# Optimization experiments

Measured on AMD Instinct MI355X. Metric: run time of the kernel, lower is better.

## Reference

```python
import jax, jax.numpy as jnp
import numpy as np

N_GENES_TOTAL = 2000
N_FREQ = 50
E_DIM = 10
N_FRAGMENTS = 131072
N_CELLS = 200
N_GENES_MB = 500
ENC_DIM = 4 * N_FREQ  # 200


def setup_inputs() -> dict:
    key = jax.random.key(0)
    k0, k1, k2, k3 = jax.random.split(key, 4)
    # fragment coordinates (start/end positions around the TSS, ~kb scale)
    coordinates = jax.random.normal(k0, (N_FRAGMENTS, 2), dtype=jnp.float32) * 1000.0
    # sorted ragged cell-x-gene segment index (required by segment_*_coo)
    local_cellxgene_ix = jnp.sort(
        jax.random.randint(k1, (N_FRAGMENTS,), 0, N_CELLS * N_GENES_MB)
    )
    # genes of interest in this minibatch (indices into the global gene table)
    genes_oi = jax.random.randint(k2, (N_GENES_MB,), 0, N_GENES_TOTAL)
    # consistent per-fragment gene mapping
    genemapping = genes_oi[local_cellxgene_ix % N_GENES_MB]
    # FragmentEmbedder params
    stdv = 1.0 / np.sqrt(E_DIM)
    W1 = jax.random.uniform(k3, (N_GENES_TOTAL, ENC_DIM, E_DIM), dtype=jnp.float32,
                            minval=-stdv, maxval=stdv)
    b1 = jnp.zeros((N_GENES_TOTAL, E_DIM), dtype=jnp.float32)
    # EmbeddingToExpression params, 'default' init: first 5 ones, rest zero, last -1
    w2 = np.zeros((N_GENES_TOTAL, E_DIM), dtype=np.float32)
    w2[:, :5] = 1.0
    w2[:, -1] = -1.0
    w2 = jnp.asarray(w2)
    b2 = jnp.zeros((N_GENES_TOTAL,), dtype=jnp.float32)
    return dict(coordinates=coordinates, genemapping=genemapping,
                local_cellxgene_ix=local_cellxgene_ix, genes_oi=genes_oi,
                W1=W1, b1=b1, w2=w2, b2=b2, cell_n=N_CELLS, gene_n=N_GENES_MB)


def _sine_encode(coordinates):
    nf = N_FREQ
    i = jnp.arange(1, nf + 1, dtype=coordinates.dtype)
    freqs = jnp.repeat(1.0 / (1000.0 ** (2.0 * i / nf)), 2)            # [2*nf]
    shifts = jnp.tile(jnp.array([0.0, jnp.pi / 2], coordinates.dtype), nf)  # [2*nf]
    # [F,2,1]*[2nf] -> [F,2,2nf] -> flatten last two -> [F, 4*nf]
    enc = jnp.sin((coordinates[..., None] * freqs + shifts)
                  .reshape(coordinates.shape[0], -1))
    return enc


def reference(coordinates, genemapping, local_cellxgene_ix, genes_oi,
              W1, b1, w2, b2, cell_n, gene_n):
    # FragmentEmbedder: sine encoding + per-gene linear + sigmoid
    enc = _sine_encode(coordinates)                                   # [F, 200]
    h = jnp.einsum('fe,feo->fo', enc, W1[genemapping]) + b1[genemapping]  # [F, 10]
    h = jax.nn.sigmoid(h)
    # EmbeddingGenePooler: segment-sum over sorted cellxgene index
    pooled = jax.ops.segment_sum(h, local_cellxgene_ix,
                                 num_segments=cell_n * gene_n,
                                 indices_are_sorted=True)             # [C*G, 10]
    pooled = pooled.reshape(cell_n, gene_n, -1)                       # [C, G, 10]
    # EmbeddingToExpression: per-gene weighted sum + bias
    out = (pooled * w2[genes_oi]).sum(-1) + b2[genes_oi]              # [C, G]
    return out
```

## Files before the change

### kernel.cpp

```cpp
#include <hip/hip_runtime.h>

#define NFRAG   131072
#define NCELLS  200
#define NGENES  500
#define NSEG    (NCELLS * NGENES)
#define EDIM    10
#define NFREQ   50
#define W1_ROW  2000
#define BLOCK   256
#define NWAVE   (BLOCK / 64)
#define CHUNKS  2
#define CPC     (NCELLS / CHUNKS)
#define MAXT    288
#define KSTEPS  7

typedef __attribute__((ext_vector_type(8))) short short8;
typedef __attribute__((ext_vector_type(4))) int   int4v;
typedef __attribute__((ext_vector_type(4))) float float4v;

__device__ inline unsigned bf16u(float f) {
    unsigned u = __float_as_uint(f);
    u += 0x7fffu + ((u >> 16) & 1u);
    return u >> 16;
}

__global__ __launch_bounds__(256) void bounds_kernel(
    const int* __restrict__ cxg, int* __restrict__ off)
{
    int f = blockIdx.x * 256 + threadIdx.x;
    if (f >= NFRAG) return;
    int cur = cxg[f];
    int nxt = (f + 1 < NFRAG) ? cxg[f + 1] : NSEG;
    if (f == 0)
        for (int s = 0; s <= cur; ++s) off[s] = 0;
    for (int s = cur + 1; s <= nxt; ++s) off[s] = f + 1;
}

__global__ __launch_bounds__(BLOCK) void gene_kernel(
    const float* __restrict__ coords,
    const int*   __restrict__ off,
    const int*   __restrict__ genes_oi,
    const float* __restrict__ W1,
    const float* __restrict__ b1,
    const float* __restrict__ w2,
    const float* __restrict__ b2,
    float* __restrict__ out)
{
    __shared__ __attribute__((aligned(16))) float sW[W1_ROW];
    __shared__ __attribute__((aligned(16))) float2 sCo[MAXT];
    __shared__ float outacc[CPC];
    __shared__ unsigned short fcell[MAXT];
    __shared__ int wtot[NWAVE + 1];

    const int g     = blockIdx.x >> 1;
    const int cbase = (blockIdx.x & 1) * CPC;
    const int t    = threadIdx.x;
    const int lane = t & 63;
    const int wid  = t >> 6;
    const int n    = lane & 15;
    const int qb   = (lane >> 4) * 8;
    const int gg   = genes_oi[g];

    int lo = 0, cnt = 0;
    if (t < CPC) {
        int seg = (cbase + t) * NGENES + g;
        int2 o2 = *((const int2*)(off + seg));
        lo  = o2.x;
        cnt = o2.y - o2.x;
    }
    const float4* Wg4 = (const float4*)(W1 + (size_t)gg * W1_ROW);
    float4 wst0 = Wg4[t];
    float4 wst1 = Wg4[t + BLOCK];
    ((float4*)sW)[t] = wst0;
    ((float4*)sW)[t + BLOCK] = wst1;
    if (t < CPC) outacc[t] = 0.0f;

    const float b1v = (n < EDIM) ? b1[gg * EDIM + n] : 0.0f;
    const float w2v = (n < EDIM) ? w2[gg * EDIM + n] : 0.0f;

    int x = cnt;
    #pragma unroll
    for (int d = 1; d < 64; d <<= 1) {
        int y = __shfl_up(x, d, 64);
        if (lane >= d) x += y;
    }
    if (lane == 63) wtot[wid] = x;
    __syncthreads();
    if (t == 0) {
        int s = 0;
        #pragma unroll
        for (int w = 0; w < NWAVE; ++w) { int v = wtot[w]; wtot[w] = s; s += v; }
        wtot[NWAVE] = s;
    }
    __syncthreads();
    int base = wtot[wid] + (x - cnt);
    const int Tfull = wtot[NWAVE];
    const int T = (Tfull < MAXT) ? Tfull : MAXT;

    for (int i = 0; i < cnt; ++i) {
        int slot = base + i;
        if (slot < MAXT) {
            sCo[slot] = ((const float2*)coords)[lo + i];
            fcell[slot] = (unsigned short)t;
        }
    }

    short8 Bf[KSTEPS];
    #pragma unroll
    for (int ks = 0; ks < KSTEPS; ++ks) {
        short8 bv;
        #pragma unroll
        for (int j = 0; j < 8; ++j) {
            int e = qb + j + 32 * ks;
            float w = (e < 200 && n < EDIM) ? sW[e * EDIM + n] : 0.0f;
            bv[j] = (short)bf16u(w);
        }
        Bf[ks] = bv;
    }

    float frv[KSTEPS * 4];
    #pragma unroll
    for (int ks = 0; ks < KSTEPS; ++ks) {
        #pragma unroll
        for (int p = 0; p < 4; ++p) {
            int e0 = qb + 32 * ks + 2 * p;
            int jj = e0; if (jj >= 200) jj -= 200; if (jj >= 100) jj -= 100;
            int kf = jj >> 1;
            frv[ks * 4 + p] = exp2f(-(float)(kf + 1) * (9.965784284662087f / 25.0f))
                              * 0.15915494309189535f;
        }
    }
    __syncthreads();

    const int tiles = (T + 15) >> 4;
    for (int tile = wid; tile < tiles; tile += NWAVE) {
        const int tb = tile << 4;
        int i = tb + n;
        if (i >= T) i = T - 1;
        float2 co = sCo[i];

        float4v acc = { b1v, b1v, b1v, b1v };

        #pragma unroll
        for (int ks = 0; ks < KSTEPS; ++ks) {
            int4v ai;
            #pragma unroll
            for (int p = 0; p < 4; ++p) {
                int e0 = qb + 32 * ks + 2 * p;
                float rev = ((e0 >= 100) ? co.y : co.x) * frv[ks * 4 + p];
                float s = __builtin_amdgcn_sinf(__builtin_amdgcn_fractf(rev));
                float c = __builtin_amdgcn_sinf(__builtin_amdgcn_fractf(rev + 0.25f));
                ai[p] = (int)(bf16u(s) | (bf16u(c) << 16));
            }
            acc = __builtin_amdgcn_mfma_f32_16x16x32_bf16(
                *(short8*)&ai, Bf[ks], acc, 0, 0, 0);
        }

        #pragma unroll
        for (int r = 0; r < 4; ++r) {
            float h = 1.0f / (1.0f + __expf(-acc[r]));
            float sv = h * w2v;
            sv += __shfl_xor(sv, 1);
            sv += __shfl_xor(sv, 2);
            sv += __shfl_xor(sv, 4);
            sv += __shfl_xor(sv, 8);
            int row = (lane >> 4) * 4 + r;
            int idx = tb + row;
            if (n == 0 && idx < T) {
                atomicAdd(&outacc[fcell[idx]], sv);
            }
        }
    }
    __syncthreads();

    if (t < CPC) out[(cbase + t) * NGENES + g] = outacc[t] + b2[gg];
}

extern "C" void kernel_launch(void* const* d_in, const int* in_sizes, int n_in,
                              void* d_out, int out_size, void* d_ws, size_t ws_size,
                              hipStream_t stream)
{
    const float* coords   = (const float*)d_in[0];
    const int*   cxg      = (const int*)  d_in[2];
    const int*   genes_oi = (const int*)  d_in[3];
    const float* W1       = (const float*)d_in[4];
    const float* b1       = (const float*)d_in[5];
    const float* w2       = (const float*)d_in[6];
    const float* b2       = (const float*)d_in[7];
    float* out = (float*)d_out;
    int*   off = (int*)d_ws;

    bounds_kernel<<<(NFRAG + 255) / 256, 256, 0, stream>>>(cxg, off);
    gene_kernel<<<NGENES * CHUNKS, BLOCK, 0, stream>>>(coords, off, genes_oi,
                                                       W1, b1, w2, b2, out);
}
```

Measured before the change: 100.9 us.

## Replace segment-offset prepass with in-kernel galloping binary search

```diff
diff --git a/kernel.cpp b/kernel.cpp
--- a/kernel.cpp
+++ b/kernel.cpp
@@ -24,21 +24,35 @@
     return u >> 16;
 }
 
-__global__ __launch_bounds__(256) void bounds_kernel(
-    const int* __restrict__ cxg, int* __restrict__ off)
-{
-    int f = blockIdx.x * 256 + threadIdx.x;
-    if (f >= NFRAG) return;
-    int cur = cxg[f];
-    int nxt = (f + 1 < NFRAG) ? cxg[f + 1] : NSEG;
-    if (f == 0)
-        for (int s = 0; s <= cur; ++s) off[s] = 0;
-    for (int s = cur + 1; s <= nxt; ++s) off[s] = f + 1;
+__device__ inline int lb_gallop(const int* __restrict__ cxg, int target) {
+    int p = (int)(((long long)target * NFRAG) / NSEG);
+    if (p > NFRAG - 1) p = NFRAG - 1;
+    if (p < 0) p = 0;
+    int lo, hi;
+    if (cxg[p] < target) {
+        int step = 256; lo = p + 1;
+        for (;;) {
+            int q = p + step;
+            if (q >= NFRAG)            { hi = NFRAG; break; }
+            if (cxg[q] >= target)      { hi = q; break; }
+            lo = q + 1; step <<= 1;
+        }
+    } else {
+        int step = 256; hi = p;
+        for (;;) {
+            int q = p - step;
+            if (q < 0)                 { lo = 0; break; }
+            if (cxg[q] < target)       { lo = q + 1; break; }
+            hi = q; step <<= 1;
+        }
+    }
+    while (lo < hi) { int m = (lo + hi) >> 1; if (cxg[m] < target) lo = m + 1; else hi = m; }
+    return lo;
 }
 
 __global__ __launch_bounds__(BLOCK) void gene_kernel(
     const float* __restrict__ coords,
-    const int*   __restrict__ off,
+    const int*   __restrict__ cxg,
     const int*   __restrict__ genes_oi,
     const float* __restrict__ W1,
     const float* __restrict__ b1,
@@ -50,6 +64,7 @@
     __shared__ __attribute__((aligned(16))) float2 sCo[MAXT];
     __shared__ float outacc[CPC];
     __shared__ unsigned short fcell[MAXT];
+    __shared__ int slo[CPC], shi[CPC];
     __shared__ int wtot[NWAVE + 1];
 
     const int g     = blockIdx.x >> 1;
@@ -61,19 +76,23 @@
     const int qb   = (lane >> 4) * 8;
     const int gg   = genes_oi[g];
 
-    int lo = 0, cnt = 0;
-    if (t < CPC) {
-        int seg = (cbase + t) * NGENES + g;
-        int2 o2 = *((const int2*)(off + seg));
-        lo  = o2.x;
-        cnt = o2.y - o2.x;
-    }
     const float4* Wg4 = (const float4*)(W1 + (size_t)gg * W1_ROW);
     float4 wst0 = Wg4[t];
     float4 wst1 = Wg4[t + BLOCK];
+
+    if (t < 2 * CPC) {
+        int cell = (t < CPC) ? t : (t - CPC);
+        int seg  = (cbase + cell) * NGENES + g + ((t < CPC) ? 0 : 1);
+        int r = lb_gallop(cxg, seg);
+        if (t < CPC) slo[cell] = r; else shi[cell] = r;
+    }
     ((float4*)sW)[t] = wst0;
     ((float4*)sW)[t + BLOCK] = wst1;
     if (t < CPC) outacc[t] = 0.0f;
+    __syncthreads();
+
+    int lo = 0, cnt = 0;
+    if (t < CPC) { lo = slo[t]; cnt = shi[t] - lo; }
 
     const float b1v = (n < EDIM) ? b1[gg * EDIM + n] : 0.0f;
     const float w2v = (n < EDIM) ? w2[gg * EDIM + n] : 0.0f;
@@ -188,9 +207,7 @@
     const float* w2       = (const float*)d_in[6];
     const float* b2       = (const float*)d_in[7];
     float* out = (float*)d_out;
-    int*   off = (int*)d_ws;
-
-    bounds_kernel<<<(NFRAG + 255) / 256, 256, 0, stream>>>(cxg, off);
-    gene_kernel<<<NGENES * CHUNKS, BLOCK, 0, stream>>>(coords, off, genes_oi,
+
+    gene_kernel<<<NGENES * CHUNKS, BLOCK, 0, stream>>>(coords, cxg, genes_oi,
                                                        W1, b1, w2, b2, out);
 }
```

After: 103.4 us. 2.5% more time.
